# Kernel optimization log

Measured on AMD Instinct MI355X. Metric: run time of the kernel, lower is better.

Reference implementation:

```python
import jax, jax.numpy as jnp
import numpy as np

D = 1024
HS = 64
NH = D // HS


def setup_inputs() -> dict:
    key = jax.random.key(0)
    ks = jax.random.split(key, 8)
    B, S = 2, 2048
    x = jax.random.normal(ks[0], (B, S, D), dtype=jnp.float32)
    y = jax.random.normal(ks[1], (B, S, D), dtype=jnp.float32)
    pad_mask = jax.random.randint(ks[2], (B, S), 0, 2).astype(jnp.int32)
    sc = 1.0 / np.sqrt(D)
    Wq = jax.random.normal(ks[3], (D, D), dtype=jnp.float32) * sc
    Wk = jax.random.normal(ks[4], (D, D), dtype=jnp.float32) * sc
    Wv = jax.random.normal(ks[5], (D, D), dtype=jnp.float32) * sc
    Wp = jax.random.normal(ks[6], (D, D), dtype=jnp.float32) * sc
    bp = jnp.zeros((D,), dtype=jnp.float32)
    return {"x": x, "y": y, "pad_mask": pad_mask, "Wq": Wq, "Wk": Wk, "Wv": Wv, "Wp": Wp, "bp": bp}


def reference(x, y, pad_mask, Wq, Wk, Wv, Wp, bp):
    B, S, _ = x.shape
    # torch Linear: out = in @ W.T  (bias=False for q/k/v)
    q = (y @ Wq.T).reshape(B, S, NH, HS).transpose(0, 2, 1, 3)  # [B,H,S,hs]
    k = (x @ Wk.T).reshape(B, S, NH, HS).transpose(0, 2, 1, 3)
    v = (x @ Wv.T).reshape(B, S, NH, HS).transpose(0, 2, 1, 3)
    att = jnp.einsum('bhqd,bhkd->bhqk', q, k) * (HS ** -0.5)  # [B,H,S,S]
    att = jnp.where((pad_mask == 0)[:, None, None, :], -jnp.inf, att)
    att = jax.nn.softmax(att, axis=-1)
    out = jnp.einsum('bhqk,bhkd->bhqd', att, v)  # [B,H,S,hs]
    out = out.transpose(0, 2, 1, 3).reshape(B, S, D)
    return out @ Wp.T + bp
```

## Files before the change

kernel.cpp:

```cpp
#include <hip/hip_runtime.h>
#include <hip/hip_bf16.h>
#include <stdint.h>

typedef unsigned short u16;
typedef unsigned int u32;
typedef float __attribute__((ext_vector_type(4))) f32x4;
typedef __bf16 __attribute__((ext_vector_type(8))) bfrag;
typedef u16 __attribute__((ext_vector_type(8))) u16x8;

#define DEV static __device__ __forceinline__

DEV u16 f2bf(float f) {
  union { float f; u32 u; } c; c.f = f;
  u32 u = c.u;
  u += 0x7fffu + ((u >> 16) & 1u);
  return (u16)(u >> 16);
}

DEV u16 bf16bits(float f) {
  __hip_bfloat16 h = __float2bfloat16(f);
  return *reinterpret_cast<u16*>(&h);
}

DEV float exp2a(float x) { return __builtin_amdgcn_exp2f(x); }

typedef const u32 __attribute__((address_space(1)))* gas_t;
typedef u32 __attribute__((address_space(3)))* las_t;

DEV void async16(const void* g, void* l) {
  __builtin_amdgcn_global_load_lds((gas_t)(uintptr_t)g, (las_t)(uintptr_t)l, 16, 0, 0);
}

__global__ __launch_bounds__(256) void convert_all(
    const float* __restrict__ x, const float* __restrict__ y,
    const float* __restrict__ wq, const float* __restrict__ wk,
    const float* __restrict__ wv, const float* __restrict__ wp,
    u16* __restrict__ xb, u16* __restrict__ yb,
    u16* __restrict__ wqb, u16* __restrict__ wkb,
    u16* __restrict__ wvb, u16* __restrict__ wpb) {
  const int NX4 = (2 * 2048 * 1024) / 4;
  const int NW4 = (1024 * 1024) / 4;
  const int total = 2 * NX4 + 4 * NW4;
  for (int i = blockIdx.x * blockDim.x + threadIdx.x; i < total;
       i += gridDim.x * blockDim.x) {
    const float4* s; ushort4* d; int off;
    if (i < NX4) { s = (const float4*)x; d = (ushort4*)xb; off = i; }
    else if (i < 2 * NX4) { s = (const float4*)y; d = (ushort4*)yb; off = i - NX4; }
    else {
      int k = i - 2 * NX4; int wsel = k >> 18; off = k & (NW4 - 1);
      s = (const float4*)(wsel == 0 ? wq : wsel == 1 ? wk : wsel == 2 ? wv : wp);
      d = (ushort4*)(wsel == 0 ? wqb : wsel == 1 ? wkb : wsel == 2 ? wvb : wpb);
    }
    float4 v = s[off];
    ushort4 o; o.x = f2bf(v.x); o.y = f2bf(v.y); o.z = f2bf(v.z); o.w = f2bf(v.w);
    d[off] = o;
  }
}

__global__ __launch_bounds__(256, 3) void gemm_qkv(
    const u16* __restrict__ xb, const u16* __restrict__ yb,
    const u16* __restrict__ wqb, const u16* __restrict__ wkb,
    const u16* __restrict__ wvb,
    u16* __restrict__ Qb, u16* __restrict__ Kb2, u16* __restrict__ Vtb) {
  const int Kd = 1024, Nd = 1024;
  __shared__ __align__(16) u16 Als[128 * 32];
  __shared__ __align__(16) u16 Bls[128 * 32];
  __shared__ __align__(16) u16 Tls[4][64 * 72];

  const int gid = blockIdx.x;
  const int seg = gid >> 8;
  const int bb = gid & 255;
  const int m0 = (bb >> 3) * 128, n0 = (bb & 7) * 128;
  const u16* A  = (seg == 0) ? yb : xb;
  const u16* Bw = (seg == 0) ? wqb : (seg == 1 ? wkb : wvb);

  const int t = threadIdx.x;
  const int lane = t & 63, w = t >> 6;
  const int wr = w >> 1, wc = w & 1;
  const int r15 = lane & 15, g = lane >> 4;
  const int rs = t >> 2, sg = t & 3;

  f32x4 acc[4][4] = {{}};
  const u16* ga = A + (size_t)(m0 + rs) * Kd + sg * 8;
  const u16* gb = Bw + (size_t)(n0 + rs) * Kd + sg * 8;

  for (int k0 = 0; k0 < Kd; k0 += 32) {
    async16(ga + k0, &Als[t * 8]);
    async16(ga + 64 * Kd + k0, &Als[(t + 256) * 8]);
    async16(gb + k0, &Bls[t * 8]);
    async16(gb + 64 * Kd + k0, &Bls[(t + 256) * 8]);
    __syncthreads();
    bfrag af[4], bfr[4];
#pragma unroll
    for (int i = 0; i < 4; i++)
      af[i] = *(const bfrag*)&Als[(wr * 64 + i * 16 + r15) * 32 + g * 8];
#pragma unroll
    for (int i = 0; i < 4; i++)
      bfr[i] = *(const bfrag*)&Bls[(wc * 64 + i * 16 + r15) * 32 + g * 8];
#pragma unroll
    for (int i = 0; i < 4; i++)
#pragma unroll
      for (int j = 0; j < 4; j++)
        acc[i][j] = __builtin_amdgcn_mfma_f32_16x16x32_bf16(af[i], bfr[j], acc[i][j], 0, 0, 0);
    __syncthreads();
  }

  if (seg < 2) {
    u16* C = (seg == 0) ? Qb : Kb2;
    const float scale = (seg == 0) ? 0.18033688f : 1.0f;
#pragma unroll
    for (int i = 0; i < 4; i++) {
#pragma unroll
      for (int j = 0; j < 4; j++) {
        int col = n0 + wc * 64 + j * 16 + r15;
        int row = m0 + wr * 64 + i * 16 + g * 4;
#pragma unroll
        for (int r = 0; r < 4; r++)
          C[(size_t)(row + r) * Nd + col] = f2bf(acc[i][j][r] * scale);
      }
    }
  } else {
#pragma unroll
    for (int i = 0; i < 4; i++)
#pragma unroll
      for (int j = 0; j < 4; j++)
#pragma unroll
        for (int r = 0; r < 4; r++)
          Tls[w][(j * 16 + r15) * 72 + (i * 16 + g * 4 + r)] = f2bf(acc[i][j][r]);
#pragma unroll
    for (int it = 0; it < 8; ++it) {
      int slot = lane + it * 64;
      int nl = slot >> 3, sgm = slot & 7;
      int4 vrow = *(const int4*)&Tls[w][nl * 72 + sgm * 8];
      int col = n0 + wc * 64 + nl;
      int h = col >> 6, hs = col & 63;
      int rowg = m0 + wr * 64 + sgm * 8;
      int b = rowg >> 11, s = rowg & 2047;
      *(int4*)&Vtb[(((size_t)b * 16 + h) * 64 + hs) * 2048 + s] = vrow;
    }
  }
}

__global__ __launch_bounds__(256, 2) void gemm_proj(
    const u16* __restrict__ A, const u16* __restrict__ Bw,
    float* __restrict__ C, const float* __restrict__ bias) {
  const int Kd = 1024, Nd = 1024;
  __shared__ __align__(16) u16 Als[64 * 32];
  __shared__ __align__(16) u16 Bls[128 * 32];
  const int t = threadIdx.x;
  const int lane = t & 63, w = t >> 6;
  const int wr = w >> 1, wc = w & 1;
  const int r15 = lane & 15, g = lane >> 4;
  const int m0 = blockIdx.y * 64, n0 = blockIdx.x * 128;
  const int rs = t >> 2, sg = t & 3;

  f32x4 acc[2][4] = {{}};
  const u16* ga = A + (size_t)(m0 + rs) * Kd + sg * 8;
  const u16* gb = Bw + (size_t)(n0 + rs) * Kd + sg * 8;

  for (int k0 = 0; k0 < Kd; k0 += 32) {
    async16(ga + k0, &Als[t * 8]);
    async16(gb + k0, &Bls[t * 8]);
    async16(gb + 64 * Kd + k0, &Bls[(t + 256) * 8]);
    __syncthreads();
    bfrag af[2], bfr[4];
#pragma unroll
    for (int i = 0; i < 2; i++)
      af[i] = *(const bfrag*)&Als[(wr * 32 + i * 16 + r15) * 32 + g * 8];
#pragma unroll
    for (int j = 0; j < 4; j++)
      bfr[j] = *(const bfrag*)&Bls[(wc * 64 + j * 16 + r15) * 32 + g * 8];
#pragma unroll
    for (int i = 0; i < 2; i++)
#pragma unroll
      for (int j = 0; j < 4; j++)
        acc[i][j] = __builtin_amdgcn_mfma_f32_16x16x32_bf16(af[i], bfr[j], acc[i][j], 0, 0, 0);
    __syncthreads();
  }

#pragma unroll
  for (int i = 0; i < 2; i++) {
#pragma unroll
    for (int j = 0; j < 4; j++) {
      int col = n0 + wc * 64 + j * 16 + r15;
      int row = m0 + wr * 32 + i * 16 + g * 4;
      float bv = bias[col];
#pragma unroll
      for (int r = 0; r < 4; r++)
        C[(size_t)(row + r) * Nd + col] = acc[i][j][r] + bv;
    }
  }
}

__global__ __launch_bounds__(256, 2) void attn_fwd(
    const u16* __restrict__ Q, const u16* __restrict__ Kb,
    const u16* __restrict__ Vt, const int* __restrict__ mask,
    u16* __restrict__ O) {
  __shared__ __align__(16) u16 Kls[2][64 * 64];
  __shared__ __align__(16) u16 Vls[2][64 * 64];
  __shared__ __align__(16) u16 Pls[4][32 * 64];
  __shared__ float biasl[2][64];

  const int bid = blockIdx.x;
  const int swz = (bid & 7) * 64 + (bid >> 3);
  const int qblk = swz & 15, bh = swz >> 4;
  const int b = bh >> 4, h = bh & 15;
  const int t = threadIdx.x, lane = t & 63, w = t >> 6;
  const int r15 = lane & 15, g = lane >> 4;
  const int qbase = qblk * 128 + w * 32;

  bfrag aQ[2][2];
  {
    const u16* Qg = Q + ((size_t)b * 2048 + qbase) * 1024 + h * 64;
#pragma unroll
    for (int mf = 0; mf < 2; ++mf)
#pragma unroll
      for (int ks = 0; ks < 2; ++ks)
        aQ[mf][ks] = *(const bfrag*)&Qg[(size_t)(mf * 16 + r15) * 1024 + ks * 32 + g * 8];
  }

  bfrag ones;
  {
    u16x8 ob = {0x3F80, 0x3F80, 0x3F80, 0x3F80, 0x3F80, 0x3F80, 0x3F80, 0x3F80};
    ones = *(bfrag*)&ob;
  }

  f32x4 oacc[2][4] = {};
  f32x4 osum[2] = {};

  const u16* Kg = Kb + (size_t)b * 2048 * 1024 + h * 64;
  const u16* Vg = Vt + (size_t)bh * 64 * 2048;
  const int* mg = mask + b * 2048;

  const int rdx = (r15 & 7) << 3;

  const int srow = t >> 3;
  const int scol = (((t & 7) ^ (srow & 7)) * 8);

  auto stage_async = [&](int kv0, int buf) {
    async16(&Kg[(size_t)(kv0 + srow) * 1024 + scol],        &Kls[buf][t * 8]);
    async16(&Kg[(size_t)(kv0 + 32 + srow) * 1024 + scol],   &Kls[buf][2048 + t * 8]);
    async16(&Vg[(size_t)srow * 2048 + kv0 + scol],          &Vls[buf][t * 8]);
    async16(&Vg[(size_t)(32 + srow) * 2048 + kv0 + scol],   &Vls[buf][2048 + t * 8]);
  };

  stage_async(0, 0);
  if (t < 64) biasl[0][t] = mg[t] ? 0.f : -1e30f;
  __syncthreads();

  float nbias = 0.f;
  for (int kt = 0; kt < 32; ++kt) {
    const int cur = kt & 1;
    if (kt < 31) {
      stage_async((kt + 1) * 64, cur ^ 1);
      if (t < 64) nbias = mg[(kt + 1) * 64 + t] ? 0.f : -1e30f;
    }

    f32x4 sc[2][4] = {};
    __builtin_amdgcn_s_setprio(1);
#pragma unroll
    for (int ks = 0; ks < 2; ++ks) {
      const int cb = (ks * 32 + g * 8) ^ rdx;
#pragma unroll
      for (int nf = 0; nf < 4; ++nf) {
        bfrag bK = *(const bfrag*)&Kls[cur][(nf * 16 + r15) * 64 + cb];
#pragma unroll
        for (int mf = 0; mf < 2; ++mf)
          sc[mf][nf] = __builtin_amdgcn_mfma_f32_16x16x32_bf16(aQ[mf][ks], bK, sc[mf][nf], 0, 0, 0);
      }
    }
    __builtin_amdgcn_s_setprio(0);

    float bcol[4];
#pragma unroll
    for (int nf = 0; nf < 4; ++nf) bcol[nf] = biasl[cur][nf * 16 + r15];

#pragma unroll
    for (int mf = 0; mf < 2; ++mf)
#pragma unroll
      for (int i = 0; i < 4; i++) {
        const int prow = mf * 16 + g * 4 + i;
        const int pxr = (prow & 7) << 3;
        u16* pr = &Pls[w][prow * 64];
#pragma unroll
        for (int nf = 0; nf < 4; ++nf) {
          float p = exp2a(sc[mf][nf][i] + bcol[nf]);
          pr[(nf * 16 + r15) ^ pxr] = bf16bits(p);
        }
      }

    __builtin_amdgcn_s_setprio(1);
#pragma unroll
    for (int ks = 0; ks < 2; ++ks) {
      const int cb = (ks * 32 + g * 8) ^ rdx;
      bfrag aP[2];
#pragma unroll
      for (int mf = 0; mf < 2; ++mf)
        aP[mf] = *(const bfrag*)&Pls[w][(mf * 16 + r15) * 64 + cb];
#pragma unroll
      for (int nf = 0; nf < 4; ++nf) {
        bfrag bV = *(const bfrag*)&Vls[cur][(nf * 16 + r15) * 64 + cb];
#pragma unroll
        for (int mf = 0; mf < 2; ++mf)
          oacc[mf][nf] = __builtin_amdgcn_mfma_f32_16x16x32_bf16(aP[mf], bV, oacc[mf][nf], 0, 0, 0);
      }
#pragma unroll
      for (int mf = 0; mf < 2; ++mf)
        osum[mf] = __builtin_amdgcn_mfma_f32_16x16x32_bf16(aP[mf], ones, osum[mf], 0, 0, 0);
    }
    __builtin_amdgcn_s_setprio(0);

    if (kt < 31 && t < 64) biasl[cur ^ 1][t] = nbias;
    __syncthreads();
  }

  u16* Og = O + ((size_t)b * 2048 + qbase) * 1024 + h * 64;
#pragma unroll
  for (int mf = 0; mf < 2; ++mf)
#pragma unroll
    for (int i = 0; i < 4; i++) {
      float rl = 1.f / osum[mf][i];
      size_t ro = (size_t)(mf * 16 + g * 4 + i) * 1024;
#pragma unroll
      for (int nf = 0; nf < 4; ++nf)
        Og[ro + nf * 16 + r15] = f2bf(oacc[mf][nf][i] * rl);
    }
}

extern "C" void kernel_launch(void* const* d_in, const int* in_sizes, int n_in,
                              void* d_out, int out_size, void* d_ws, size_t ws_size,
                              hipStream_t stream) {
  const float* x  = (const float*)d_in[0];
  const float* y  = (const float*)d_in[1];
  const int*  msk = (const int*)d_in[2];
  const float* Wq = (const float*)d_in[3];
  const float* Wk = (const float*)d_in[4];
  const float* Wv = (const float*)d_in[5];
  const float* Wp = (const float*)d_in[6];
  const float* bp = (const float*)d_in[7];

  char* ws = (char*)d_ws;
  const size_t SZ_XB = (size_t)2 * 2048 * 1024 * 2;
  const size_t SZ_W  = (size_t)1024 * 1024 * 2;
  u16* xb  = (u16*)(ws);
  u16* yb  = (u16*)(ws + SZ_XB);
  u16* wqb = (u16*)(ws + 2 * SZ_XB);
  u16* wkb = (u16*)(ws + 2 * SZ_XB + SZ_W);
  u16* wvb = (u16*)(ws + 2 * SZ_XB + 2 * SZ_W);
  u16* wpb = (u16*)(ws + 2 * SZ_XB + 3 * SZ_W);
  u16* Qb  = (u16*)(ws + 2 * SZ_XB + 4 * SZ_W);
  u16* Kb2 = (u16*)(ws + 3 * SZ_XB + 4 * SZ_W);
  u16* Vtb = (u16*)(ws + 4 * SZ_XB + 4 * SZ_W);
  u16* Ob  = (u16*)(ws + 5 * SZ_XB + 4 * SZ_W);

  convert_all<<<2048, 256, 0, stream>>>(x, y, Wq, Wk, Wv, Wp, xb, yb, wqb, wkb, wvb, wpb);
  gemm_qkv<<<768, 256, 0, stream>>>(xb, yb, wqb, wkb, wvb, Qb, Kb2, Vtb);
  attn_fwd<<<512, 256, 0, stream>>>(Qb, Kb2, Vtb, msk, Ob);
  dim3 gg(8, 64);
  gemm_proj<<<gg, 256, 0, stream>>>(Ob, wpb, (float*)d_out, bp);
}
```

Before: 125.1 us.

## Double GEMM K-step to 64 with XOR-swizzled LDS tiles in QKV and proj

Both GEMM kernels now stage 64-wide K slices per barrier pair instead of 32, halving the number of __syncthreads per GEMM. LDS tiles use an XOR swizzle on 16-byte column chunks so fragment reads avoid bank conflicts. In the QKV kernel the transpose scratch buffer is aliased onto the same LDS arena to keep shared memory usage bounded. LDS per block grows, which may reduce occupancy for gemm_proj.

```diff
diff --git a/kernel.cpp b/kernel.cpp
--- a/kernel.cpp
+++ b/kernel.cpp
@@ -63,9 +63,9 @@
     const u16* __restrict__ wvb,
     u16* __restrict__ Qb, u16* __restrict__ Kb2, u16* __restrict__ Vtb) {
   const int Kd = 1024, Nd = 1024;
-  __shared__ __align__(16) u16 Als[128 * 32];
-  __shared__ __align__(16) u16 Bls[128 * 32];
-  __shared__ __align__(16) u16 Tls[4][64 * 72];
+  __shared__ __align__(16) u16 arena[18432];
+  u16* Als = arena;
+  u16* Bls = arena + 8192;
 
   const int gid = blockIdx.x;
   const int seg = gid >> 8;
@@ -78,30 +78,38 @@
   const int lane = t & 63, w = t >> 6;
   const int wr = w >> 1, wc = w & 1;
   const int r15 = lane & 15, g = lane >> 4;
-  const int rs = t >> 2, sg = t & 3;
+  const int rdx = (r15 & 7) << 3;
+
+  const int srow = t >> 3;
+  const int scol = ((t & 7) ^ (srow & 7)) * 8;
 
   f32x4 acc[4][4] = {{}};
-  const u16* ga = A + (size_t)(m0 + rs) * Kd + sg * 8;
-  const u16* gb = Bw + (size_t)(n0 + rs) * Kd + sg * 8;
-
-  for (int k0 = 0; k0 < Kd; k0 += 32) {
-    async16(ga + k0, &Als[t * 8]);
-    async16(ga + 64 * Kd + k0, &Als[(t + 256) * 8]);
-    async16(gb + k0, &Bls[t * 8]);
-    async16(gb + 64 * Kd + k0, &Bls[(t + 256) * 8]);
-    __syncthreads();
-    bfrag af[4], bfr[4];
-#pragma unroll
-    for (int i = 0; i < 4; i++)
-      af[i] = *(const bfrag*)&Als[(wr * 64 + i * 16 + r15) * 32 + g * 8];
-#pragma unroll
-    for (int i = 0; i < 4; i++)
-      bfr[i] = *(const bfrag*)&Bls[(wc * 64 + i * 16 + r15) * 32 + g * 8];
-#pragma unroll
-    for (int i = 0; i < 4; i++)
+  const u16* ga = A + (size_t)(m0 + srow) * Kd + scol;
+  const u16* gb = Bw + (size_t)(n0 + srow) * Kd + scol;
+
+  for (int k0 = 0; k0 < Kd; k0 += 64) {
+#pragma unroll
+    for (int c = 0; c < 4; ++c) {
+      async16(ga + (size_t)c * 32 * Kd + k0, &Als[c * 2048 + t * 8]);
+      async16(gb + (size_t)c * 32 * Kd + k0, &Bls[c * 2048 + t * 8]);
+    }
+    __syncthreads();
+#pragma unroll
+    for (int ks = 0; ks < 2; ++ks) {
+      const int cb = (ks * 32 + g * 8) ^ rdx;
+      bfrag af[4], bfr[4];
+#pragma unroll
+      for (int i = 0; i < 4; i++)
+        af[i] = *(const bfrag*)&Als[(wr * 64 + i * 16 + r15) * 64 + cb];
 #pragma unroll
       for (int j = 0; j < 4; j++)
-        acc[i][j] = __builtin_amdgcn_mfma_f32_16x16x32_bf16(af[i], bfr[j], acc[i][j], 0, 0, 0);
+        bfr[j] = *(const bfrag*)&Bls[(wc * 64 + j * 16 + r15) * 64 + cb];
+#pragma unroll
+      for (int i = 0; i < 4; i++)
+#pragma unroll
+        for (int j = 0; j < 4; j++)
+          acc[i][j] = __builtin_amdgcn_mfma_f32_16x16x32_bf16(af[i], bfr[j], acc[i][j], 0, 0, 0);
+    }
     __syncthreads();
   }
 
@@ -120,18 +128,19 @@
       }
     }
   } else {
+    u16* Tw = arena + w * 4608;
 #pragma unroll
     for (int i = 0; i < 4; i++)
 #pragma unroll
       for (int j = 0; j < 4; j++)
 #pragma unroll
         for (int r = 0; r < 4; r++)
-          Tls[w][(j * 16 + r15) * 72 + (i * 16 + g * 4 + r)] = f2bf(acc[i][j][r]);
+          Tw[(j * 16 + r15) * 72 + (i * 16 + g * 4 + r)] = f2bf(acc[i][j][r]);
 #pragma unroll
     for (int it = 0; it < 8; ++it) {
       int slot = lane + it * 64;
       int nl = slot >> 3, sgm = slot & 7;
-      int4 vrow = *(const int4*)&Tls[w][nl * 72 + sgm * 8];
+      int4 vrow = *(const int4*)&Tw[nl * 72 + sgm * 8];
       int col = n0 + wc * 64 + nl;
       int h = col >> 6, hs = col & 63;
       int rowg = m0 + wr * 64 + sgm * 8;
@@ -145,36 +154,45 @@
     const u16* __restrict__ A, const u16* __restrict__ Bw,
     float* __restrict__ C, const float* __restrict__ bias) {
   const int Kd = 1024, Nd = 1024;
-  __shared__ __align__(16) u16 Als[64 * 32];
-  __shared__ __align__(16) u16 Bls[128 * 32];
+  __shared__ __align__(16) u16 Als[64 * 64];
+  __shared__ __align__(16) u16 Bls[128 * 64];
   const int t = threadIdx.x;
   const int lane = t & 63, w = t >> 6;
   const int wr = w >> 1, wc = w & 1;
   const int r15 = lane & 15, g = lane >> 4;
   const int m0 = blockIdx.y * 64, n0 = blockIdx.x * 128;
-  const int rs = t >> 2, sg = t & 3;
+  const int rdx = (r15 & 7) << 3;
+  const int srow = t >> 3;
+  const int scol = ((t & 7) ^ (srow & 7)) * 8;
 
   f32x4 acc[2][4] = {{}};
-  const u16* ga = A + (size_t)(m0 + rs) * Kd + sg * 8;
-  const u16* gb = Bw + (size_t)(n0 + rs) * Kd + sg * 8;
-
-  for (int k0 = 0; k0 < Kd; k0 += 32) {
-    async16(ga + k0, &Als[t * 8]);
-    async16(gb + k0, &Bls[t * 8]);
-    async16(gb + 64 * Kd + k0, &Bls[(t + 256) * 8]);
-    __syncthreads();
-    bfrag af[2], bfr[4];
-#pragma unroll
-    for (int i = 0; i < 2; i++)
-      af[i] = *(const bfrag*)&Als[(wr * 32 + i * 16 + r15) * 32 + g * 8];
-#pragma unroll
-    for (int j = 0; j < 4; j++)
-      bfr[j] = *(const bfrag*)&Bls[(wc * 64 + j * 16 + r15) * 32 + g * 8];
-#pragma unroll
-    for (int i = 0; i < 2; i++)
+  const u16* ga = A + (size_t)(m0 + srow) * Kd + scol;
+  const u16* gb = Bw + (size_t)(n0 + srow) * Kd + scol;
+
+  for (int k0 = 0; k0 < Kd; k0 += 64) {
+#pragma unroll
+    for (int c = 0; c < 2; ++c)
+      async16(ga + (size_t)c * 32 * Kd + k0, &Als[c * 2048 + t * 8]);
+#pragma unroll
+    for (int c = 0; c < 4; ++c)
+      async16(gb + (size_t)c * 32 * Kd + k0, &Bls[c * 2048 + t * 8]);
+    __syncthreads();
+#pragma unroll
+    for (int ks = 0; ks < 2; ++ks) {
+      const int cb = (ks * 32 + g * 8) ^ rdx;
+      bfrag af[2], bfr[4];
+#pragma unroll
+      for (int i = 0; i < 2; i++)
+        af[i] = *(const bfrag*)&Als[(wr * 32 + i * 16 + r15) * 64 + cb];
 #pragma unroll
       for (int j = 0; j < 4; j++)
-        acc[i][j] = __builtin_amdgcn_mfma_f32_16x16x32_bf16(af[i], bfr[j], acc[i][j], 0, 0, 0);
+        bfr[j] = *(const bfrag*)&Bls[(wc * 64 + j * 16 + r15) * 64 + cb];
+#pragma unroll
+      for (int i = 0; i < 2; i++)
+#pragma unroll
+        for (int j = 0; j < 4; j++)
+          acc[i][j] = __builtin_amdgcn_mfma_f32_16x16x32_bf16(af[i], bfr[j], acc[i][j], 0, 0, 0);
+    }
     __syncthreads();
   }
 
@@ -233,7 +251,6 @@
   const int* mg = mask + b * 2048;
 
   const int rdx = (r15 & 7) << 3;
-
   const int srow = t >> 3;
   const int scol = (((t & 7) ^ (srow & 7)) * 8);
 
```

After: 117.6 us. 5.9% less time.
